# Optimization experiments

Measured on AMD Instinct MI355X. Metric: run time of the kernel, lower is better.

## Reference

```python
import jax, jax.numpy as jnp
import numpy as np

NEG = -1e12  # additive causal mask value used in the original TF code


def setup_inputs() -> dict:
    key = jax.random.key(0)
    k1, k2, k3, k4 = jax.random.split(key, 4)
    B, T, D, U = 4, 4096, 128, 128
    query = jax.random.normal(k1, (B, T, D), dtype=jnp.float32)
    # glorot-style scaled dense weights (no bias, matching use_bias=False)
    s = 1.0 / np.sqrt(D)
    Wq = jax.random.normal(k2, (D, U), dtype=jnp.float32) * s
    Wk = jax.random.normal(k3, (D, U), dtype=jnp.float32) * s
    Wv = jax.random.normal(k4, (D, U), dtype=jnp.float32) * s
    return {"query": query, "Wq": Wq, "Wk": Wk, "Wv": Wv}


def reference(query, Wq, Wk, Wv):
    # Self-attention path: value = key = query (pre-projection)
    q = jnp.einsum('btd,du->btu', query, Wq)
    k = jnp.einsum('btd,du->btu', query, Wk)
    v = jnp.einsum('btd,du->btu', query, Wv)
    T = v.shape[1]
    # NOTE: original scales by sqrt(seq_len) (tf.shape(value)[1]), kept faithfully
    scores = jnp.einsum('bqu,bku->bqk', q, k) / jnp.sqrt(jnp.asarray(T, jnp.float32))
    # additive causal mask: lower-triangular kept, upper gets -1e12
    causal = jnp.tril(jnp.ones((T, T), dtype=jnp.float32))
    scores = scores + NEG * (1.0 - causal)
    attn = jax.nn.softmax(scores, axis=-1)
    context = jnp.einsum('bqk,bku->bqu', attn, v)
    return context
```

## Files before the change

### kernel.cpp

```cpp
#include <hip/hip_runtime.h>

#define T_SEQ 4096
#define BATCH 4
#define DD 128
#define BT (BATCH * T_SEQ)
#define CPB 12
#define KPB 176
#define MAXPARTS 12

typedef __bf16 bf16x8 __attribute__((ext_vector_type(8)));
typedef float f32x4 __attribute__((ext_vector_type(4)));

__device__ inline bf16x8 ld8(const unsigned short* p) {
  return *reinterpret_cast<const bf16x8*>(p);
}
__device__ inline unsigned short bfc(float f) {
  __bf16 v = (__bf16)f;
  return __builtin_bit_cast(unsigned short, v);
}
__device__ inline float fexp2(float x) {
  float r;
  asm("v_exp_f32 %0, %1" : "=v"(r) : "v"(x));
  return r;
}
__device__ inline int vsw(int sIdx) {
  return sIdx ^ ((((sIdx >> 6) & 3) << 3));
}

#define MFMA(a, b, c) __builtin_amdgcn_mfma_f32_16x16x32_bf16((a), (b), (c), 0, 0, 0)

__global__ void wt_kernel(const float* __restrict__ Wq, const float* __restrict__ Wk,
                          const float* __restrict__ Wv,
                          unsigned short* __restrict__ fq, unsigned short* __restrict__ fk,
                          unsigned short* __restrict__ fv) {
  const float* W = (blockIdx.y == 0) ? Wq : (blockIdx.y == 1) ? Wk : Wv;
  unsigned short* F = (blockIdx.y == 0) ? fq : (blockIdx.y == 1) ? fk : fv;
  int e = blockIdx.x * 256 + threadIdx.x;
  int j = e & 7, lane = (e >> 3) & 63, nc = e >> 9;
  int c = nc & 3, n0 = nc >> 2;
  int t = lane & 15, g = lane >> 4;
  F[e] = bfc(W[(c * 32 + g * 8 + j) * 128 + n0 * 16 + t]);
}

__global__ __launch_bounds__(256) void proj_kernel(
    const float* __restrict__ X,
    const unsigned short* __restrict__ fq,
    const unsigned short* __restrict__ fk,
    const unsigned short* __restrict__ fv,
    unsigned short* __restrict__ qf,
    unsigned short* __restrict__ kf,
    unsigned short* __restrict__ vt) {
  const int tid = threadIdx.x;
  const int w = tid >> 6, lane = tid & 63;
  const int t = lane & 15, g = lane >> 4;
  const int r0 = blockIdx.x * 32;

  __shared__ unsigned short xs[2][16 * 136];

  bf16x8 wq[2][4], wk[2][4], wv[2][4];
#pragma unroll
  for (int s = 0; s < 2; ++s)
#pragma unroll
    for (int c = 0; c < 4; ++c) {
      int fo = (((w + s * 4) * 4 + c) * 64 + lane) * 8;
      wq[s][c] = ld8(fq + fo);
      wk[s][c] = ld8(fk + fo);
      wv[s][c] = ld8(fv + fo);
    }

#pragma unroll
  for (int sub = 0; sub < 2; ++sub) {
    int r = tid >> 4, cb = tid & 15;
    const float* xp = X + (size_t)(r0 + sub * 16 + r) * DD + cb * 8;
    float4 lo = *reinterpret_cast<const float4*>(xp);
    float4 hi = *reinterpret_cast<const float4*>(xp + 4);
    bf16x8 tmp;
    tmp[0] = (__bf16)lo.x; tmp[1] = (__bf16)lo.y; tmp[2] = (__bf16)lo.z; tmp[3] = (__bf16)lo.w;
    tmp[4] = (__bf16)hi.x; tmp[5] = (__bf16)hi.y; tmp[6] = (__bf16)hi.z; tmp[7] = (__bf16)hi.w;
    *reinterpret_cast<bf16x8*>(&xs[sub][r * 136 + cb * 8]) = tmp;
  }
  __syncthreads();

#pragma unroll
  for (int sub = 0; sub < 2; ++sub) {
    const int r0s = r0 + sub * 16;
    bf16x8 x[4];
#pragma unroll
    for (int c = 0; c < 4; ++c)
      x[c] = ld8(&xs[sub][t * 136 + c * 32 + g * 8]);

#pragma unroll
    for (int s = 0; s < 2; ++s) {
      const int n0 = w + s * 4;
      f32x4 aq = {0.f, 0.f, 0.f, 0.f}, ak = {0.f, 0.f, 0.f, 0.f};
#pragma unroll
      for (int c = 0; c < 4; ++c) {
        aq = MFMA(x[c], wq[s][c], aq);
        ak = MFMA(x[c], wk[s][c], ak);
      }
      const int cP = n0 >> 1;
      const int Gp = ((n0 & 1) << 1) | (t >> 3);
      const int ep = t & 7;
#pragma unroll
      for (int r = 0; r < 4; ++r) {
        int row = r0s + g * 4 + r;
        size_t qoff = ((size_t)((row >> 4) * 4 + cP) * 64 + ((Gp << 4) | (row & 15))) * 8 + ep;
        qf[qoff] = bfc(aq[r] * 0.0225421101f);
        int tp = (row & 3) | (((row >> 3) & 3) << 2);
        size_t koff =
            ((size_t)(((row >> 5) * 2 + ((row >> 2) & 1)) * 4 + cP) * 64 + ((Gp << 4) | tp)) * 8 +
            ep;
        kf[koff] = bfc(ak[r]);
      }
    }

    const int key = r0s + t;
    const size_t vbase = (size_t)(key >> 5) * 4096 + (key & 31);
#pragma unroll
    for (int s = 0; s < 2; ++s) {
      const int u0 = w + s * 4;
      f32x4 av = {0.f, 0.f, 0.f, 0.f};
#pragma unroll
      for (int c = 0; c < 4; ++c)
        av = MFMA(wv[s][c], x[c], av);
#pragma unroll
      for (int r = 0; r < 4; ++r)
        vt[vbase + (size_t)(u0 * 16 + g * 4 + r) * 32] = bfc(av[r]);
    }
  }
}

__global__ __launch_bounds__(256, 2) void attn_kernel(
    const unsigned short* __restrict__ qf,
    const unsigned short* __restrict__ kf,
    const unsigned short* __restrict__ vt,
    float* __restrict__ pO,
    float* __restrict__ pL,
    float* __restrict__ out) {
  const int tid = threadIdx.x;
  const int w = tid >> 6, lane = tid & 63;
  const int t = lane & 15, G = lane >> 4;
  const int bi = blockIdx.x;
  const int xcd = bi & 7;
  const int b = xcd >> 1;
  const int k = ((bi >> 3) << 1) | (xcd & 1);

  const int m0 = k * CPB, mend = m0 + CPB;
  int sg = (int)(0.5f * (sqrtf(1.0f + 2.0f * (float)m0) - 1.0f));
  while (2 * (sg + 1) * (sg + 2) <= m0) ++sg;
  while (2 * sg * (sg + 1) > m0) --sg;
  int j = m0 - 2 * sg * (sg + 1);

  const unsigned short* kfb = kf + (size_t)b * (T_SEQ * DD);
  const unsigned short* vtb = vt + (size_t)b * (T_SEQ * DD);

  __shared__ unsigned short bufK[2][4096], bufV[2][4096];

  bf16x8 st0, st1, st2, st3;
  {
    const unsigned short* kch = kfb + (size_t)j * 4096;
    const unsigned short* vch = vtb + (size_t)j * 4096;
    st0 = ld8(kch + tid * 8);
    st1 = ld8(kch + 2048 + tid * 8);
    st2 = ld8(vch + tid * 8);
    st3 = ld8(vch + 2048 + tid * 8);
    *reinterpret_cast<bf16x8*>(&bufK[0][tid * 8]) = st0;
    *reinterpret_cast<bf16x8*>(&bufK[0][2048 + tid * 8]) = st1;
    *reinterpret_cast<bf16x8*>(&bufV[0][vsw(tid * 8)]) = st2;
    *reinterpret_cast<bf16x8*>(&bufV[0][vsw(2048 + tid * 8)]) = st3;
  }
  __syncthreads();

  int sgS = sg, jS = j + 1;
  if (jS == 4 * sgS + 4) { ++sgS; jS = 0; }

  bf16x8 qa[2][4];
  f32x4 O[2][8];
  float ls0 = 0.f, ls1 = 0.f;
  bool fresh = true;
  int jbeg = j;
  int cur = 0;

  for (int m = m0; m < mend; ++m) {
    const int sig32 = 4 * sg + w;
    const int q0 = sig32 * 32;

    if (fresh) {
#pragma unroll
      for (int p = 0; p < 2; ++p)
#pragma unroll
        for (int c = 0; c < 4; ++c)
          qa[p][c] = ld8(qf + ((size_t)((b * 256 + 2 * sig32 + p) * 4 + c) * 64 + lane) * 8);
#pragma unroll
      for (int p = 0; p < 2; ++p)
#pragma unroll
        for (int u0 = 0; u0 < 8; ++u0) O[p][u0] = (f32x4){0.f, 0.f, 0.f, 0.f};
      ls0 = 0.f; ls1 = 0.f;
      jbeg = j;
      fresh = false;
    }

    const bool more = (m + 1 < mend);
    if (more) {
      const unsigned short* kch = kfb + (size_t)jS * 4096;
      const unsigned short* vch = vtb + (size_t)jS * 4096;
      st0 = ld8(kch + tid * 8);
      st1 = ld8(kch + 2048 + tid * 8);
      st2 = ld8(vch + tid * 8);
      st3 = ld8(vch + 2048 + tid * 8);
    }

    if (j <= sig32) {
      f32x4 s00 = {0.f, 0.f, 0.f, 0.f}, s01 = {0.f, 0.f, 0.f, 0.f};
      f32x4 s10 = {0.f, 0.f, 0.f, 0.f}, s11 = {0.f, 0.f, 0.f, 0.f};
      {
        bf16x8 kc[4];
#pragma unroll
        for (int c = 0; c < 4; ++c) kc[c] = ld8(&bufK[cur][c * 512 + lane * 8]);
#pragma unroll
        for (int c = 0; c < 4; ++c) {
          s00 = MFMA(kc[c], qa[0][c], s00);
          s10 = MFMA(kc[c], qa[1][c], s10);
        }
#pragma unroll
        for (int c = 0; c < 4; ++c) kc[c] = ld8(&bufK[cur][(4 + c) * 512 + lane * 8]);
#pragma unroll
        for (int c = 0; c < 4; ++c) {
          s01 = MFMA(kc[c], qa[0][c], s01);
          s11 = MFMA(kc[c], qa[1][c], s11);
        }
      }

      bf16x8 pb0, pb1;
      if (j < sig32) {
#pragma unroll
        for (int r = 0; r < 4; ++r) {
          float e00 = fexp2(s00[r]), e01 = fexp2(s01[r]);
          float e10 = fexp2(s10[r]), e11 = fexp2(s11[r]);
          ls0 += e00 + e01;
          ls1 += e10 + e11;
          pb0[r] = (__bf16)e00; pb0[r + 4] = (__bf16)e01;
          pb1[r] = (__bf16)e10; pb1[r + 4] = (__bf16)e11;
        }
      } else {
#pragma unroll
        for (int r = 0; r < 4; ++r) {
          int k0 = j * 32 + G * 8 + r;
          float e00 = (k0 <= q0 + t) ? fexp2(s00[r]) : 0.f;
          float e01 = (k0 + 4 <= q0 + t) ? fexp2(s01[r]) : 0.f;
          float e10 = (k0 <= q0 + 16 + t) ? fexp2(s10[r]) : 0.f;
          float e11 = (k0 + 4 <= q0 + 16 + t) ? fexp2(s11[r]) : 0.f;
          ls0 += e00 + e01;
          ls1 += e10 + e11;
          pb0[r] = (__bf16)e00; pb0[r + 4] = (__bf16)e01;
          pb1[r] = (__bf16)e10; pb1[r + 4] = (__bf16)e11;
        }
      }

#pragma unroll
      for (int u0 = 0; u0 < 8; ++u0) {
        bf16x8 vcu = ld8(&bufV[cur][vsw((u0 * 16 + t) * 32 + G * 8)]);
        O[0][u0] = MFMA(pb0, vcu, O[0][u0]);
        O[1][u0] = MFMA(pb1, vcu, O[1][u0]);
      }
    }

    const bool gend = (j == 4 * sg + 3);
    if (gend || m == mend - 1) {
      float r0s = ls0; r0s += __shfl_xor(r0s, 16); r0s += __shfl_xor(r0s, 32);
      float r1s = ls1; r1s += __shfl_xor(r1s, 16); r1s += __shfl_xor(r1s, 32);
      if (jbeg == 0 && gend) {
        float linv0[4], linv1[4];
#pragma unroll
        for (int r = 0; r < 4; ++r) {
          linv0[r] = 1.0f / __shfl(r0s, G * 4 + r);
          linv1[r] = 1.0f / __shfl(r1s, G * 4 + r);
        }
        float* op0 = out + ((size_t)(b * T_SEQ + q0 + G * 4)) * DD + t;
        float* op1 = op0 + (size_t)16 * DD;
#pragma unroll
        for (int u0 = 0; u0 < 8; ++u0) {
#pragma unroll
          for (int r = 0; r < 4; ++r) {
            op0[(size_t)r * DD + u0 * 16] = O[0][u0][r] * linv0[r];
            op1[(size_t)r * DD + u0 * 16] = O[1][u0][r] * linv1[r];
          }
        }
      } else {
        const int part = k - (2 * sg * (sg + 1)) / CPB;
        const int slot = (b * 128 + sig32) * MAXPARTS + part;
        if (lane < 16) {
          pL[slot * 32 + lane] = r0s;
          pL[slot * 32 + 16 + lane] = r1s;
        }
        float* pb = pO + (size_t)slot * 4096 + (size_t)(G * 4) * DD + t;
#pragma unroll
        for (int u0 = 0; u0 < 8; ++u0) {
#pragma unroll
          for (int r = 0; r < 4; ++r) {
            pb[(size_t)r * DD + u0 * 16] = O[0][u0][r];
            pb[(size_t)(16 + r) * DD + u0 * 16] = O[1][u0][r];
          }
        }
      }
      fresh = true;
    }

    if (more) {
      const int nxt = cur ^ 1;
      *reinterpret_cast<bf16x8*>(&bufK[nxt][tid * 8]) = st0;
      *reinterpret_cast<bf16x8*>(&bufK[nxt][2048 + tid * 8]) = st1;
      *reinterpret_cast<bf16x8*>(&bufV[nxt][vsw(tid * 8)]) = st2;
      *reinterpret_cast<bf16x8*>(&bufV[nxt][vsw(2048 + tid * 8)]) = st3;
    }
    __syncthreads();
    cur ^= 1;

    ++j;
    if (j == 4 * sg + 4) { ++sg; j = 0; }
    if (more) {
      ++jS;
      if (jS == 4 * sgS + 4) { ++sgS; jS = 0; }
    }
  }
}

__global__ __launch_bounds__(256) void comb_kernel(const float* __restrict__ pO,
                                                   const float* __restrict__ pL,
                                                   float* __restrict__ out) {
  const int bi = blockIdx.x;
  const int b = bi >> 7, sig32 = bi & 127;
  const int sg = sig32 >> 2;
  const int cum = 2 * sg * (sg + 1);
  const int n = 4 * sg + 4;
  const int kfirst = cum / CPB, klast = (cum + n - 1) / CPB;
  const int parts = klast - kfirst + 1;
  if (parts == 1) return;
  const int tid = threadIdx.x;
  const int q = tid >> 3, uc = (tid & 7) * 16;
  const int slot0 = (b * 128 + sig32) * MAXPARTS;

  float ls = 0.f;
  for (int p = 0; p < parts; ++p) ls += pL[(slot0 + p) * 32 + q];
  const float linv = 1.0f / ls;

  float4 acc[4] = {{0,0,0,0},{0,0,0,0},{0,0,0,0},{0,0,0,0}};
  for (int p = 0; p < parts; ++p) {
    const float* src = pO + (size_t)(slot0 + p) * 4096 + (size_t)q * DD + uc;
#pragma unroll
    for (int e = 0; e < 4; ++e) {
      float4 v = *reinterpret_cast<const float4*>(src + e * 4);
      acc[e].x += v.x; acc[e].y += v.y; acc[e].z += v.z; acc[e].w += v.w;
    }
  }
  float* dst = out + ((size_t)(b * T_SEQ + sig32 * 32 + q)) * DD + uc;
#pragma unroll
  for (int e = 0; e < 4; ++e) {
    acc[e].x *= linv; acc[e].y *= linv; acc[e].z *= linv; acc[e].w *= linv;
    *reinterpret_cast<float4*>(dst + e * 4) = acc[e];
  }
}

extern "C" void kernel_launch(void* const* d_in, const int* in_sizes, int n_in,
                              void* d_out, int out_size, void* d_ws, size_t ws_size,
                              hipStream_t stream) {
  const float* X  = (const float*)d_in[0];
  const float* Wq = (const float*)d_in[1];
  const float* Wk = (const float*)d_in[2];
  const float* Wv = (const float*)d_in[3];
  float* out = (float*)d_out;

  unsigned short* qf = (unsigned short*)d_ws;
  unsigned short* kf = qf + (size_t)BT * DD;
  unsigned short* vt = kf + (size_t)BT * DD;
  unsigned short* fq = vt + (size_t)BT * DD;
  unsigned short* fk = fq + DD * DD;
  unsigned short* fv = fk + DD * DD;
  float* pO = (float*)(fv + DD * DD);
  float* pL = pO + (size_t)BATCH * 128 * MAXPARTS * 32 * 128;

  dim3 wt_grid(64, 3);
  wt_kernel<<<wt_grid, 256, 0, stream>>>(Wq, Wk, Wv, fq, fk, fv);
  proj_kernel<<<BT / 32, 256, 0, stream>>>(X, fq, fk, fv, qf, kf, vt);
  attn_kernel<<<BATCH * KPB, 256, 0, stream>>>(qf, kf, vt, pO, pL, out);
  comb_kernel<<<512, 256, 0, stream>>>(pO, pL, out);
}
```

Measured before the change: 114.8 us.

## Replace fixed-chunk streaming split with per-query-group split-KV partitioning

Each attention block previously processed a fixed run of 12 KV chunks that could span several query groups, which needed fresh-state handling and partial outputs for every boundary crossing. Now each block owns exactly one query group and a contiguous KV range. Groups are split into 1-4 parts according to their causal length, and the largest groups are scheduled first. This removes the mid-loop flush and reload logic and reduces partial writes and combine work. The cost is fewer blocks (320 vs 704) and less even per-block load balance.

```diff
diff --git a/kernel.cpp b/kernel.cpp
--- a/kernel.cpp
+++ b/kernel.cpp
@@ -4,9 +4,7 @@
 #define BATCH 4
 #define DD 128
 #define BT (BATCH * T_SEQ)
-#define CPB 12
-#define KPB 176
-#define MAXPARTS 12
+#define MAXPARTS 4
 
 typedef __bf16 bf16x8 __attribute__((ext_vector_type(8)));
 typedef float f32x4 __attribute__((ext_vector_type(4)));
@@ -145,21 +143,44 @@
   const int b = xcd >> 1;
   const int k = ((bi >> 3) << 1) | (xcd & 1);
 
-  const int m0 = k * CPB, mend = m0 + CPB;
-  int sg = (int)(0.5f * (sqrtf(1.0f + 2.0f * (float)m0) - 1.0f));
-  while (2 * (sg + 1) * (sg + 2) <= m0) ++sg;
-  while (2 * sg * (sg + 1) > m0) --sg;
-  int j = m0 - 2 * sg * (sg + 1);
+  const int a = 79 - k;
+  int o = 0;
+  while (4 * (o + 1) * (o + 2) <= a) ++o;
+  const int idx = a - 4 * o * (o + 1);
+  const int sg = 8 * o + idx / (o + 1);
+  const int p = idx % (o + 1);
+  const int parts = o + 1;
+  const int N = 4 * sg + 4;
+  const int qn = N / parts, rem = N % parts;
+  const int jlo = p * qn + min(p, rem);
+  const int jhi = jlo + qn + (p < rem ? 1 : 0);
+
+  const int sig32 = 4 * sg + w;
+  const int q0 = sig32 * 32;
 
   const unsigned short* kfb = kf + (size_t)b * (T_SEQ * DD);
   const unsigned short* vtb = vt + (size_t)b * (T_SEQ * DD);
 
   __shared__ unsigned short bufK[2][4096], bufV[2][4096];
 
+  bf16x8 qa[2][4];
+#pragma unroll
+  for (int pp = 0; pp < 2; ++pp)
+#pragma unroll
+    for (int c = 0; c < 4; ++c)
+      qa[pp][c] = ld8(qf + ((size_t)((b * 256 + 2 * sig32 + pp) * 4 + c) * 64 + lane) * 8);
+
+  f32x4 O[2][8];
+#pragma unroll
+  for (int pp = 0; pp < 2; ++pp)
+#pragma unroll
+    for (int u0 = 0; u0 < 8; ++u0) O[pp][u0] = (f32x4){0.f, 0.f, 0.f, 0.f};
+  float ls0 = 0.f, ls1 = 0.f;
+
   bf16x8 st0, st1, st2, st3;
   {
-    const unsigned short* kch = kfb + (size_t)j * 4096;
-    const unsigned short* vch = vtb + (size_t)j * 4096;
+    const unsigned short* kch = kfb + (size_t)jlo * 4096;
+    const unsigned short* vch = vtb + (size_t)jlo * 4096;
     st0 = ld8(kch + tid * 8);
     st1 = ld8(kch + 2048 + tid * 8);
     st2 = ld8(vch + tid * 8);
@@ -171,39 +192,12 @@
   }
   __syncthreads();
 
-  int sgS = sg, jS = j + 1;
-  if (jS == 4 * sgS + 4) { ++sgS; jS = 0; }
-
-  bf16x8 qa[2][4];
-  f32x4 O[2][8];
-  float ls0 = 0.f, ls1 = 0.f;
-  bool fresh = true;
-  int jbeg = j;
   int cur = 0;
-
-  for (int m = m0; m < mend; ++m) {
-    const int sig32 = 4 * sg + w;
-    const int q0 = sig32 * 32;
-
-    if (fresh) {
-#pragma unroll
-      for (int p = 0; p < 2; ++p)
-#pragma unroll
-        for (int c = 0; c < 4; ++c)
-          qa[p][c] = ld8(qf + ((size_t)((b * 256 + 2 * sig32 + p) * 4 + c) * 64 + lane) * 8);
-#pragma unroll
-      for (int p = 0; p < 2; ++p)
-#pragma unroll
-        for (int u0 = 0; u0 < 8; ++u0) O[p][u0] = (f32x4){0.f, 0.f, 0.f, 0.f};
-      ls0 = 0.f; ls1 = 0.f;
-      jbeg = j;
-      fresh = false;
-    }
-
-    const bool more = (m + 1 < mend);
+  for (int j = jlo; j < jhi; ++j) {
+    const bool more = (j + 1 < jhi);
     if (more) {
-      const unsigned short* kch = kfb + (size_t)jS * 4096;
-      const unsigned short* vch = vtb + (size_t)jS * 4096;
+      const unsigned short* kch = kfb + (size_t)(j + 1) * 4096;
+      const unsigned short* vch = vtb + (size_t)(j + 1) * 4096;
       st0 = ld8(kch + tid * 8);
       st1 = ld8(kch + 2048 + tid * 8);
       st2 = ld8(vch + tid * 8);
@@ -265,62 +259,50 @@
       }
     }
 
-    const bool gend = (j == 4 * sg + 3);
-    if (gend || m == mend - 1) {
-      float r0s = ls0; r0s += __shfl_xor(r0s, 16); r0s += __shfl_xor(r0s, 32);
-      float r1s = ls1; r1s += __shfl_xor(r1s, 16); r1s += __shfl_xor(r1s, 32);
-      if (jbeg == 0 && gend) {
-        float linv0[4], linv1[4];
-#pragma unroll
-        for (int r = 0; r < 4; ++r) {
-          linv0[r] = 1.0f / __shfl(r0s, G * 4 + r);
-          linv1[r] = 1.0f / __shfl(r1s, G * 4 + r);
-        }
-        float* op0 = out + ((size_t)(b * T_SEQ + q0 + G * 4)) * DD + t;
-        float* op1 = op0 + (size_t)16 * DD;
-#pragma unroll
-        for (int u0 = 0; u0 < 8; ++u0) {
-#pragma unroll
-          for (int r = 0; r < 4; ++r) {
-            op0[(size_t)r * DD + u0 * 16] = O[0][u0][r] * linv0[r];
-            op1[(size_t)r * DD + u0 * 16] = O[1][u0][r] * linv1[r];
-          }
-        }
-      } else {
-        const int part = k - (2 * sg * (sg + 1)) / CPB;
-        const int slot = (b * 128 + sig32) * MAXPARTS + part;
-        if (lane < 16) {
-          pL[slot * 32 + lane] = r0s;
-          pL[slot * 32 + 16 + lane] = r1s;
-        }
-        float* pb = pO + (size_t)slot * 4096 + (size_t)(G * 4) * DD + t;
-#pragma unroll
-        for (int u0 = 0; u0 < 8; ++u0) {
-#pragma unroll
-          for (int r = 0; r < 4; ++r) {
-            pb[(size_t)r * DD + u0 * 16] = O[0][u0][r];
-            pb[(size_t)(16 + r) * DD + u0 * 16] = O[1][u0][r];
-          }
-        }
-      }
-      fresh = true;
-    }
-
     if (more) {
       const int nxt = cur ^ 1;
       *reinterpret_cast<bf16x8*>(&bufK[nxt][tid * 8]) = st0;
       *reinterpret_cast<bf16x8*>(&bufK[nxt][2048 + tid * 8]) = st1;
       *reinterpret_cast<bf16x8*>(&bufV[nxt][vsw(tid * 8)]) = st2;
       *reinterpret_cast<bf16x8*>(&bufV[nxt][vsw(2048 + tid * 8)]) = st3;
-    }
-    __syncthreads();
-    cur ^= 1;
-
-    ++j;
-    if (j == 4 * sg + 4) { ++sg; j = 0; }
-    if (more) {
-      ++jS;
-      if (jS == 4 * sgS + 4) { ++sgS; jS = 0; }
+      __syncthreads();
+      cur ^= 1;
+    }
+  }
+
+  float r0s = ls0; r0s += __shfl_xor(r0s, 16); r0s += __shfl_xor(r0s, 32);
+  float r1s = ls1; r1s += __shfl_xor(r1s, 16); r1s += __shfl_xor(r1s, 32);
+  if (parts == 1) {
+    float linv0[4], linv1[4];
+#pragma unroll
+    for (int r = 0; r < 4; ++r) {
+      linv0[r] = 1.0f / __shfl(r0s, G * 4 + r);
+      linv1[r] = 1.0f / __shfl(r1s, G * 4 + r);
+    }
+    float* op0 = out + ((size_t)(b * T_SEQ + q0 + G * 4)) * DD + t;
+    float* op1 = op0 + (size_t)16 * DD;
+#pragma unroll
+    for (int u0 = 0; u0 < 8; ++u0) {
+#pragma unroll
+      for (int r = 0; r < 4; ++r) {
+        op0[(size_t)r * DD + u0 * 16] = O[0][u0][r] * linv0[r];
+        op1[(size_t)r * DD + u0 * 16] = O[1][u0][r] * linv1[r];
+      }
+    }
+  } else {
+    const int slot = (b * 128 + sig32) * MAXPARTS + p;
+    if (lane < 16) {
+      pL[slot * 32 + lane] = r0s;
+      pL[slot * 32 + 16 + lane] = r1s;
+    }
+    float* pb = pO + (size_t)slot * 4096 + (size_t)(G * 4) * DD + t;
+#pragma unroll
+    for (int u0 = 0; u0 < 8; ++u0) {
+#pragma unroll
+      for (int r = 0; r < 4; ++r) {
+        pb[(size_t)r * DD + u0 * 16] = O[0][u0][r];
+        pb[(size_t)(16 + r) * DD + u0 * 16] = O[1][u0][r];
+      }
     }
   }
 }
@@ -331,10 +313,7 @@
   const int bi = blockIdx.x;
   const int b = bi >> 7, sig32 = bi & 127;
   const int sg = sig32 >> 2;
-  const int cum = 2 * sg * (sg + 1);
-  const int n = 4 * sg + 4;
-  const int kfirst = cum / CPB, klast = (cum + n - 1) / CPB;
-  const int parts = klast - kfirst + 1;
+  const int parts = sg / 8 + 1;
   if (parts == 1) return;
   const int tid = threadIdx.x;
   const int q = tid >> 3, uc = (tid & 7) * 16;
@@ -382,6 +361,6 @@
   dim3 wt_grid(64, 3);
   wt_kernel<<<wt_grid, 256, 0, stream>>>(Wq, Wk, Wv, fq, fk, fv);
   proj_kernel<<<BT / 32, 256, 0, stream>>>(X, fq, fk, fv, qf, kf, vt);
-  attn_kernel<<<BATCH * KPB, 256, 0, stream>>>(qf, kf, vt, pO, pL, out);
+  attn_kernel<<<320, 256, 0, stream>>>(qf, kf, vt, pO, pL, out);
   comb_kernel<<<512, 256, 0, stream>>>(pO, pL, out);
 }
```

Result: no change. 116.3 us (+1.3%).
